# Performance work log

Measured on AMD Instinct MI355X. Metric: run time of the kernel, lower is better.

The kernel has to match this reference:

```python
import jax, jax.numpy as jnp
import numpy as np

LMAX = 6; MMAX = 2
C = 128          # num_channels
H = 8            # num_heads
ALPHA = 32       # attn_alpha_channels
VAL = 16         # attn_value_channels (H*VAL == C)
HID = 64         # attn_hidden_channels
FFN = 128        # ffn_hidden_channels
NL = 4           # num_layers
CUTOFF = 12.0; NRBF = 600
AVG_DEG = 23.395238876342773
AVG_NODES = 77.81317
EPS = 1e-16

def _maps():
    idx, ls = [], []
    for l in range(LMAX + 1):
        mm = min(l, MMAX)
        for m in range(-mm, mm + 1):
            idx.append(l * l + l + m); ls.append(l)
    return np.array(idx), np.array(ls)
_M2F_np, _LOF_np = _maps()
M2F = jnp.asarray(_M2F_np)   # [KM] full-coefficient index of each m-restricted coeff
LOF = jnp.asarray(_LOF_np)   # [KM] degree l of each m-restricted coeff
KM = int(_M2F_np.shape[0])   # 29 for lmax=6, mmax=2
KF = (LMAX + 1) ** 2         # 49

def _rbf(d):
    # GaussianSmearing(0, cutoff, NRBF, width_scalar=2.0)
    off = jnp.linspace(0.0, CUTOFF, NRBF)
    coeff = -0.5 / (2.0 * (off[1] - off[0])) ** 2
    return jnp.exp(coeff * (d[:, None] - off) ** 2)

def _envelope(d):
    # PolynomialEnvelope, exponent p=5
    x = d / CUTOFF
    env = 1.0 - 21.0 * x ** 5 + 35.0 * x ** 6 - 15.0 * x ** 7
    return jnp.where(x < 1.0, env, 0.0)

def _rms(x, g):
    # merge-norm over channel dim with learned per-channel scale
    return x * jax.lax.rsqrt(jnp.mean(x * x, axis=-1, keepdims=True) + 1e-6) * g

def _forward(atomic_numbers, edge_index, edge_distance, emb,
             We0, be0, We1, be1, Weproj, gamma1, gamma2,
             Wr0, Wr1, Wrl, Wmsg, Wap, wa, Wg, Wv, Wo,
             Wf1, Wfg, Wf2, Wh1, Wh2):
    N = atomic_numbers.shape[0]
    src, tgt = edge_index[0], edge_index[1]
    rbf = _rbf(edge_distance)            # [E, NRBF]
    env = _envelope(edge_distance)       # [E]
    # node init: atom embedding on the l=0 component
    x = jnp.zeros((N, KF, C), rbf.dtype).at[:, 0, :].set(emb[atomic_numbers])
    # edge-degree embedding: radial MLP -> per-edge coeffs -> scatter to targets
    h = jax.nn.silu(rbf @ We0 + be0)
    h = jax.nn.silu(h @ We1 + be1)
    deg = (h @ Weproj).reshape(-1, KM, C)              # [E, KM, C]
    x = x.at[tgt[:, None], M2F[None, :], :].add(deg / AVG_DEG)
    for i in range(NL):
        # ---- equivariant graph attention ----
        y = _rms(x, gamma1[i])
        ym = y[:, M2F, :]                               # [N, KM, C] m-restricted
        m = jnp.concatenate([ym[src], ym[tgt]], axis=-1)  # [E, KM, 2C]
        m = jnp.einsum('ekc,ch->ekh', m, Wmsg[i])       # [E, KM, HID]
        # radial function, shared across m within each l (use_rad_l_parametrization)
        rad = jax.nn.silu(jax.nn.silu(rbf @ Wr0[i]) @ Wr1[i])
        radl = rad @ Wrl[i]                             # [E, LMAX+1]
        m = m * radl[:, LOF][..., None]
        # attention logits from invariant (l=0) part
        a = jax.nn.silu(m[:, 0, :] @ Wap[i]).reshape(-1, H, ALPHA)
        logits = jnp.einsum('eha,ha->eh', a, wa[i])     # [E, H]
        segmax = jnp.full((N, H), -jnp.inf, logits.dtype).at[tgt].max(logits)
        ex = env[:, None] * jnp.exp(logits - segmax[tgt])  # envelope-masked softmax
        den = jax.ops.segment_sum(ex, tgt, num_segments=N)
        attn = ex / (den[tgt] + EPS)                    # [E, H]
        # SwiGLU-gated equivariant values
        g = jax.nn.silu(m[:, 0, :] @ Wg[i])             # [E, H*VAL]
        v = jnp.einsum('ekh,hv->ekv', m, Wv[i]) * g[:, None, :]
        v = v.reshape(-1, KM, H, VAL) * attn[:, None, :, None]
        agg = jax.ops.segment_sum(v.reshape(-1, KM, H * VAL), tgt, num_segments=N)
        out = jnp.einsum('nkv,vc->nkc', agg, Wo[i])     # [N, KM, C]
        x = x.at[:, M2F, :].add(out)
        # ---- feed-forward (grid-MLP style SwiGLU) ----
        y = _rms(x, gamma2[i])
        gf = jax.nn.silu(y[:, 0, :] @ Wfg[i])           # [N, FFN]
        hf = jnp.einsum('nkc,cf->nkf', y, Wf1[i]) * gf[:, None, :]
        x = x + jnp.einsum('nkf,fc->nkc', hf, Wf2[i])
    # energy head on invariant part, sum-aggregated over nodes
    s = jax.nn.silu(x[:, 0, :] @ Wh1) @ Wh2             # [N, 1]
    return (jnp.sum(s) / AVG_NODES).reshape(1)

def setup_inputs() -> dict:
    key = jax.random.key(0)
    ks = jax.random.split(key, 24)
    N, E = 6000, 120000
    def rn(k, shape, scale=0.05):
        return jax.random.normal(k, shape, dtype=jnp.float32) * scale
    inp = {}
    inp['atomic_numbers'] = jax.random.randint(ks[0], (N,), 0, 128)
    inp['edge_index'] = jax.random.randint(ks[1], (2, E), 0, N)
    inp['edge_distance'] = jax.random.uniform(ks[2], (E,), minval=0.5, maxval=CUTOFF, dtype=jnp.float32)
    inp['emb'] = rn(ks[3], (128, C), 1.0)
    inp['We0'] = rn(ks[4], (NRBF, 128)); inp['be0'] = jnp.zeros((128,), jnp.float32)
    inp['We1'] = rn(ks[5], (128, 128)); inp['be1'] = jnp.zeros((128,), jnp.float32)
    inp['Weproj'] = rn(ks[6], (128, KM * C))
    inp['gamma1'] = jnp.ones((NL, C), jnp.float32)
    inp['gamma2'] = jnp.ones((NL, C), jnp.float32)
    inp['Wr0'] = rn(ks[7], (NL, NRBF, 128))
    inp['Wr1'] = rn(ks[8], (NL, 128, 128))
    inp['Wrl'] = rn(ks[9], (NL, 128, LMAX + 1), 0.1)
    inp['Wmsg'] = rn(ks[10], (NL, 2 * C, HID))
    inp['Wap'] = rn(ks[11], (NL, HID, H * ALPHA))
    inp['wa'] = rn(ks[12], (NL, H, ALPHA))
    inp['Wg'] = rn(ks[13], (NL, HID, H * VAL))
    inp['Wv'] = rn(ks[14], (NL, HID, H * VAL))
    inp['Wo'] = rn(ks[15], (NL, H * VAL, C))
    inp['Wf1'] = rn(ks[16], (NL, C, FFN))
    inp['Wfg'] = rn(ks[17], (NL, C, FFN))
    inp['Wf2'] = rn(ks[18], (NL, FFN, C))
    inp['Wh1'] = rn(ks[19], (C, C))
    inp['Wh2'] = rn(ks[20], (C, 1))
    return inp

def reference(atomic_numbers, edge_index, edge_distance, emb,
              We0, be0, We1, be1, Weproj, gamma1, gamma2,
              Wr0, Wr1, Wrl, Wmsg, Wap, wa, Wg, Wv, Wo,
              Wf1, Wfg, Wf2, Wh1, Wh2):
    return _forward(atomic_numbers, edge_index, edge_distance, emb,
                    We0, be0, We1, be1, Weproj, gamma1, gamma2,
                    Wr0, Wr1, Wrl, Wmsg, Wap, wa, Wg, Wv, Wo,
                    Wf1, Wfg, Wf2, Wh1, Wh2)
```

## Files before the change

kernel.cpp:

```cpp
#include <hip/hip_runtime.h>

#define KM 29
#define GTAB 2048

typedef __bf16 bf16_t;
typedef __bf16 bf16x8 __attribute__((ext_vector_type(8)));
typedef __bf16 bf16x4 __attribute__((ext_vector_type(4)));
typedef __bf16 bf16x2 __attribute__((ext_vector_type(2)));
typedef float  f32x4  __attribute__((ext_vector_type(4)));
typedef float  f32x2  __attribute__((ext_vector_type(2)));

__device__ __forceinline__ float silu_f(float x){ return x / (1.0f + __expf(-x)); }

__device__ __forceinline__ float wave_reduce_sum(float v){
  #pragma unroll
  for (int s = 1; s < 64; s <<= 1) v += __shfl_xor(v, s);
  return v;
}

__device__ __forceinline__ constexpr int LOF2(int k){
  return (k<1)?0 : (k<4)?1 : (k<9)?2 : (k<14)?3 : (k<19)?4 : (k<24)?5 : 6;
}

__device__ __forceinline__ f32x4 mfma16(bf16x8 a, bf16x8 b, f32x4 c){
  return __builtin_amdgcn_mfma_f32_16x16x32_bf16(a, b, c, 0, 0, 0);
}

__device__ __forceinline__ float env_f(float d){
  float xx = d*(1.0f/12.0f);
  float x2 = xx*xx, x4 = x2*x2, x5 = x4*xx;
  float env = 1.0f - 21.0f*x5 + 35.0f*x5*xx - 15.0f*x5*x2;
  return (xx < 1.0f) ? env : 0.0f;
}

__global__ void k_count(const int* __restrict__ EI, int* __restrict__ cnt, int E){
  int e = blockIdx.x*256 + threadIdx.x;
  if (e < E) atomicAdd(&cnt[EI[E+e]], 1);
}

__global__ __launch_bounds__(1024) void k_scan(int* __restrict__ cnt, int* __restrict__ rowptr, int N){
  __shared__ int ts[1024];
  int t = threadIdx.x;
  int base = t*8;
  int loc[8]; int sum = 0;
  #pragma unroll
  for (int u = 0; u < 8; u++){ int idx = base+u; int v = (idx < N) ? cnt[idx] : 0; loc[u] = sum; sum += v; }
  ts[t] = sum; __syncthreads();
  for (int off = 1; off < 1024; off <<= 1){
    int v = (t >= off) ? ts[t-off] : 0;
    __syncthreads();
    ts[t] += v;
    __syncthreads();
  }
  int excl = ts[t] - sum;
  #pragma unroll
  for (int u = 0; u < 8; u++){
    int idx = base+u;
    if (idx < N){ int r = excl + loc[u]; rowptr[idx] = r; cnt[idx] = r; }
  }
  if (t == 1023) rowptr[N] = ts[1023];
}

__global__ void k_fill(const int* __restrict__ EI, int* __restrict__ cur, int* __restrict__ order, int E){
  int e = blockIdx.x*256 + threadIdx.x;
  if (e < E){ int pos = atomicAdd(&cur[EI[E+e]], 1); order[pos] = e; }
}

__global__ void k_sort(const int* __restrict__ rowptr, int* __restrict__ order, int N){
  int n = blockIdx.x*256 + threadIdx.x;
  if (n >= N) return;
  int rp = rowptr[n], re = rowptr[n+1];
  for (int a = rp+1; a < re; a++){
    int key = order[a]; int b = a-1;
    while (b >= rp && order[b] > key){ order[b+1] = order[b]; b--; }
    order[b+1] = key;
  }
}

__global__ void k_tr(const float* __restrict__ src, bf16_t* __restrict__ dst,
                     int L, int R, int C, int Lstr){
  int idx = blockIdx.x*256 + threadIdx.x;
  int total = L*R*C;
  if (idx >= total) return;
  int l = idx / (R*C); int rem = idx - l*(R*C);
  int r = rem / C; int c = rem - r*C;
  dst[((size_t)l*C + c)*R + r] = (bf16_t)src[(size_t)l*Lstr + (size_t)r*C + c];
}

__global__ void k_tr2(const float* __restrict__ src, bf16_t* __restrict__ dst){
  int idx = blockIdx.x*256 + threadIdx.x;
  if (idx >= 4*128*128) return;
  int l = idx >> 14; int j = (idx >> 7) & 127; int c = idx & 127;
  float v = (j < 64) ? src[(size_t)l*16384 + c*64 + j]
                     : src[(size_t)l*16384 + 8192 + c*64 + (j-64)];
  dst[idx] = (bf16_t)v;
}

__global__ __launch_bounds__(256) void k_tab_embed(
    const float* __restrict__ We0, const float* __restrict__ be0,
    const float* __restrict__ We1, const float* __restrict__ be1,
    const float* __restrict__ Wr0, const float* __restrict__ Wr1, const float* __restrict__ Wrl,
    float* __restrict__ h2tab, float* __restrict__ radtab)
{
  __shared__ float sb[4][640];
  const int wid = threadIdx.x >> 6, lane = threadIdx.x & 63;
  const int e = blockIdx.x*4 + wid;
  if (e >= GTAB) return;
  const float d = e * (12.0f/(GTAB-1));
  const float DLT = 12.0f/599.0f;
  const float CO  = -0.5f/((2.0f*DLT)*(2.0f*DLT));
  int jc = (int)(d/DLT + 0.5f);
  int j0 = jc - 16; if (j0 < 0) j0 = 0; if (j0 > 600-32) j0 = 600-32;
  float diff = d - (float)(j0+lane)*DLT;
  float gval = __expf(CO*diff*diff);
  float p[10];
  #pragma unroll
  for (int u = 0; u < 10; u++) p[u] = 0.f;
  const int c2 = 2*lane;
  for (int jj = 0; jj < 32; jj++){
    float gj = __shfl(gval, jj);
    int row = j0 + jj;
    const float2 w0 = *(const float2*)(We0 + row*128 + c2);
    p[0] += gj*w0.x; p[1] += gj*w0.y;
    #pragma unroll
    for (int i = 0; i < 4; i++){
      const float2 wr = *(const float2*)(Wr0 + ((size_t)i*600 + row)*128 + c2);
      p[2+2*i] += gj*wr.x; p[3+2*i] += gj*wr.y;
    }
  }
  sb[wid][c2]   = silu_f(p[0] + be0[c2]);
  sb[wid][c2+1] = silu_f(p[1] + be0[c2+1]);
  #pragma unroll
  for (int i = 0; i < 4; i++){
    sb[wid][128 + 128*i + c2]   = silu_f(p[2+2*i]);
    sb[wid][128 + 128*i + c2+1] = silu_f(p[3+2*i]);
  }
  float a0 = 0.f, a1 = 0.f;
  for (int c = 0; c < 128; c++){
    float hv = sb[wid][c];
    const float2 w = *(const float2*)(We1 + c*128 + c2);
    a0 += hv*w.x; a1 += hv*w.y;
  }
  a0 = silu_f(a0 + be1[c2]); a1 = silu_f(a1 + be1[c2+1]);
  h2tab[(size_t)e*128 + c2]     = a0;
  h2tab[(size_t)e*128 + c2 + 1] = a1;
  #pragma unroll
  for (int i = 0; i < 4; i++){
    float r0 = 0.f, r1 = 0.f;
    const float* W1 = Wr1 + (size_t)i*128*128;
    for (int c = 0; c < 128; c++){
      float rv = sb[wid][128 + 128*i + c];
      const float2 w = *(const float2*)(W1 + c*128 + c2);
      r0 += rv*w.x; r1 += rv*w.y;
    }
    r0 = silu_f(r0); r1 = silu_f(r1);
    const float* Wl = Wrl + (size_t)i*128*7;
    float pl[7];
    #pragma unroll
    for (int l = 0; l < 7; l++) pl[l] = r0*Wl[c2*7+l] + r1*Wl[(c2+1)*7+l];
    #pragma unroll
    for (int l = 0; l < 7; l++) pl[l] = wave_reduce_sum(pl[l]);
    if (lane == 0){
      #pragma unroll
      for (int l = 0; l < 7; l++) radtab[(size_t)e*28 + i*7 + l] = pl[l];
    }
  }
}

__global__ void k_h2e(const float* __restrict__ ed, const float* __restrict__ h2tab,
                      bf16_t* __restrict__ h2e, int E){
  int idx = blockIdx.x*256 + threadIdx.x;
  if (idx >= E*128) return;
  int e = idx >> 7, ch = idx & 127;
  float d = ed[e];
  float u = d * ((GTAB-1)/12.0f);
  int j = (int)u; if (j > GTAB-2) j = GTAB-2;
  float f = u - (float)j;
  float a = h2tab[(size_t)j*128 + ch], b = h2tab[(size_t)(j+1)*128 + ch];
  h2e[idx] = (bf16_t)(a + f*(b-a));
}

__global__ __launch_bounds__(256) void k_init_x(
    const int* __restrict__ Z, const float* __restrict__ emb,
    const bf16_t* __restrict__ WeprojT, const bf16_t* __restrict__ h2e,
    const int* __restrict__ rowptr, const int* __restrict__ order,
    bf16_t* __restrict__ Xb, int N)
{
  __shared__ bf16_t h2s[32*136];
  __shared__ int Zs[32];
  int n0 = blockIdx.x*32, t = threadIdx.x;
  int half = t >> 7, ch = t & 127;
  for (int pair = 0; pair < 16; pair++){
    int nn = pair*2 + half;
    int n = n0 + nn;
    float acc = 0.f;
    if (n < N){
      int rp = rowptr[n], deg = rowptr[n+1]-rp;
      for (int idx = 0; idx < deg; idx++){
        int e = order[rp+idx];
        acc += (float)h2e[(size_t)e*128 + ch];
      }
    }
    h2s[nn*136 + ch] = (bf16_t)acc;
  }
  if (t < 32) Zs[t] = (n0 + t < N) ? Z[n0+t] : 0;
  __syncthreads();
  int wid = t >> 6, lane = t & 63;
  int mtile = wid & 1;
  int row = mtile*16 + (lane & 15);
  int koff = (lane >> 4)*8;
  bf16x8 afr[4];
  #pragma unroll
  for (int kk = 0; kk < 4; kk++) afr[kk] = *(const bf16x8*)(h2s + row*136 + kk*32 + koff);
  for (int nt = (wid>>1); nt < 232; nt += 2){
    f32x4 acc = {0.f,0.f,0.f,0.f};
    int col = nt*16 + (lane & 15);
    #pragma unroll
    for (int kk = 0; kk < 4; kk++){
      bf16x8 b = *(const bf16x8*)(WeprojT + (size_t)col*128 + kk*32 + koff);
      acc = mfma16(afr[kk], b, acc);
    }
    #pragma unroll
    for (int r = 0; r < 4; r++){
      int r32 = mtile*16 + (lane>>4)*4 + r;
      int n = n0 + r32;
      if (n < N){
        float v = acc[r] * (1.0f/23.395238876342773f);
        if (col < 128) v += emb[(size_t)Zs[r32]*128 + col];
        Xb[(size_t)n*3712 + col] = (bf16_t)v;
      }
    }
  }
}

__global__ __launch_bounds__(512) void k_pqv(
    const bf16_t* __restrict__ Xb, const float* __restrict__ gamma1,
    const bf16_t* __restrict__ WmsgCT, const bf16_t* __restrict__ WvT,
    unsigned char* __restrict__ PV8, bf16_t* __restrict__ qmb,
    float* __restrict__ P0, float* __restrict__ Q0, int layer)
{
  __shared__ bf16_t ys16[32*136];
  __shared__ bf16_t pq16[32*136];
  int n = blockIdx.x, t = threadIdx.x;
  int wid = t >> 6, lane = t & 63;
  const float* g1 = gamma1 + layer*128;
  const bf16_t* xp = Xb + (size_t)n*3712;
  for (int k = wid; k < KM; k += 8){
    float x0 = (float)xp[k*128 + lane], x1 = (float)xp[k*128 + 64 + lane];
    float ss = wave_reduce_sum(x0*x0 + x1*x1);
    float sc = rsqrtf(ss*(1.0f/128.0f) + 1e-6f);
    ys16[k*136 + lane]      = (bf16_t)(x0*sc*g1[lane]);
    ys16[k*136 + 64 + lane] = (bf16_t)(x1*sc*g1[64+lane]);
  }
  for (int idx = t; idx < 3*136; idx += 512) ys16[29*136 + idx] = (bf16_t)0.f;
  __syncthreads();
  int mtile = wid >> 2;
  int row = mtile*16 + (lane & 15);
  int koff = (lane >> 4)*8;
  {
    const bf16_t* Bc = WmsgCT + (size_t)layer*16384;
    f32x4 acc[2] = {{0,0,0,0},{0,0,0,0}};
    #pragma unroll
    for (int kk = 0; kk < 128; kk += 32){
      bf16x8 a = *(const bf16x8*)(ys16 + row*136 + kk + koff);
      #pragma unroll
      for (int u = 0; u < 2; u++){
        int col = ((wid&3)*2+u)*16 + (lane & 15);
        bf16x8 b = *(const bf16x8*)(Bc + (size_t)col*128 + kk + koff);
        acc[u] = mfma16(a, b, acc[u]);
      }
    }
    #pragma unroll
    for (int u = 0; u < 2; u++){
      int col = ((wid&3)*2+u)*16 + (lane & 15);
      #pragma unroll
      for (int r = 0; r < 4; r++){
        int r32 = mtile*16 + (lane>>4)*4 + r;
        pq16[r32*136 + col] = (bf16_t)acc[u][r];
      }
      if (mtile == 0 && (lane>>4) == 0){
        float v = acc[u][0];
        if (col < 64) P0[(size_t)n*64 + col] = v;
        else          Q0[(size_t)n*64 + col - 64] = v;
      }
    }
  }
  __syncthreads();
  {
    const bf16_t* Bt = WvT + (size_t)layer*8192;
    f32x4 acc[2] = {{0,0,0,0},{0,0,0,0}};
    #pragma unroll
    for (int kk = 0; kk < 64; kk += 32){
      bf16x8 a = *(const bf16x8*)(pq16 + row*136 + kk + koff);
      #pragma unroll
      for (int u = 0; u < 2; u++){
        int col = ((wid&3)*2+u)*16 + (lane & 15);
        bf16x8 b = *(const bf16x8*)(Bt + (size_t)col*64 + kk + koff);
        acc[u] = mfma16(a, b, acc[u]);
      }
    }
    unsigned char* pvp = PV8 + (size_t)n*4096;
    int r0i = mtile*16 + (lane>>4)*4;
    #pragma unroll
    for (int u = 0; u < 2; u++){
      int col = ((wid&3)*2+u)*16 + (lane & 15);
      float pk[4];
      #pragma unroll
      for (int r = 0; r < 4; r++){
        int r32 = r0i + r;
        pk[r] = (r32 < KM) ? acc[u][r] : 0.f;
      }
      int dw = __builtin_amdgcn_cvt_pk_fp8_f32(pk[0], pk[1], 0, false);
      dw = __builtin_amdgcn_cvt_pk_fp8_f32(pk[2], pk[3], dw, true);
      *(unsigned int*)(pvp + col*32 + r0i) = (unsigned int)dw;
    }
  }
  for (int idx = t; idx < KM*64; idx += 512){
    int k = idx >> 6, j = idx & 63;
    qmb[(size_t)n*1856 + idx] = pq16[k*136 + 64 + j];
  }
}

__global__ __launch_bounds__(256) void k_edge_logits(
    const int* __restrict__ EI, const float* __restrict__ ed,
    const float* __restrict__ P0, const float* __restrict__ Q0,
    const float* __restrict__ radtab, const bf16_t* __restrict__ WapT, const float* __restrict__ wa,
    const bf16_t* __restrict__ WgT, float* __restrict__ logi, bf16_t* __restrict__ gate16,
    int E, int layer)
{
  __shared__ bf16_t m0s[16*72];
  __shared__ int   srcs[16], tgts[16];
  __shared__ float r0s[16];
  int t = threadIdx.x;
  int eb = blockIdx.x*16;
  if (t < 16){
    int e = eb + t;
    if (e < E){
      srcs[t] = EI[e]; tgts[t] = EI[E+e];
      float d = ed[e];
      float u = d * ((GTAB-1)/12.0f);
      int j = (int)u; if (j > GTAB-2) j = GTAB-2;
      float f = u - (float)j;
      float a = radtab[(size_t)j*28 + layer*7], b = radtab[(size_t)(j+1)*28 + layer*7];
      r0s[t] = a + f*(b-a);
    } else { srcs[t] = 0; tgts[t] = 0; r0s[t] = 0.f; }
  }
  __syncthreads();
  #pragma unroll
  for (int u = 0; u < 4; u++){
    int idx = t + u*256;
    int i = idx >> 6, j = idx & 63;
    m0s[i*72 + j] = (bf16_t)((P0[(size_t)srcs[i]*64 + j] + Q0[(size_t)tgts[i]*64 + j]) * r0s[i]);
  }
  __syncthreads();
  int wid = t >> 6, lane = t & 63;
  int l15 = lane & 15, lg = lane >> 4;
  int koff = lg*8;
  bf16x8 a0 = *(const bf16x8*)(m0s + l15*72 + koff);
  bf16x8 a1 = *(const bf16x8*)(m0s + l15*72 + 32 + koff);
  const bf16_t* Ba = WapT + (size_t)layer*16384;
  const bf16_t* Bg = WgT  + (size_t)layer*8192;
  const float* wav = wa + layer*256;
  f32x4 accA[4], accG[2];
  #pragma unroll
  for (int u = 0; u < 4; u++){
    int col = 64*wid + u*16 + l15;
    f32x4 acc = {0,0,0,0};
    acc = mfma16(a0, *(const bf16x8*)(Ba + (size_t)col*64 + koff), acc);
    acc = mfma16(a1, *(const bf16x8*)(Ba + (size_t)col*64 + 32 + koff), acc);
    accA[u] = acc;
  }
  #pragma unroll
  for (int u = 0; u < 2; u++){
    int col = 32*wid + u*16 + l15;
    f32x4 acc = {0,0,0,0};
    acc = mfma16(a0, *(const bf16x8*)(Bg + (size_t)col*64 + koff), acc);
    acc = mfma16(a1, *(const bf16x8*)(Bg + (size_t)col*64 + 32 + koff), acc);
    accG[u] = acc;
  }
  #pragma unroll
  for (int u = 0; u < 2; u++){
    int col = 32*wid + u*16 + l15;
    #pragma unroll
    for (int r = 0; r < 4; r++){
      int e = eb + lg*4 + r;
      if (e < E) gate16[(size_t)e*128 + col] = (bf16_t)silu_f(accG[u][r]);
    }
  }
  #pragma unroll
  for (int hpair = 0; hpair < 2; hpair++){
    int c0 = 64*wid + hpair*32 + l15;
    float w0 = wav[c0], w1 = wav[c0+16];
    float s[4];
    #pragma unroll
    for (int r = 0; r < 4; r++)
      s[r] = silu_f(accA[2*hpair][r])*w0 + silu_f(accA[2*hpair+1][r])*w1;
    #pragma unroll
    for (int r = 0; r < 4; r++){
      s[r] += __shfl_xor(s[r], 1);
      s[r] += __shfl_xor(s[r], 2);
      s[r] += __shfl_xor(s[r], 4);
      s[r] += __shfl_xor(s[r], 8);
    }
    if (l15 == 0){
      #pragma unroll
      for (int r = 0; r < 4; r++){
        int e = eb + lg*4 + r;
        if (e < E) logi[(size_t)e*8 + 2*wid + hpair] = s[r];
      }
    }
  }
}

#define FMA_DW(dw, kb) { \
  f32x2 lo_ = __builtin_amdgcn_cvt_pk_f32_fp8((dw), false); \
  f32x2 hi_ = __builtin_amdgcn_cvt_pk_f32_fp8((dw), true); \
  acc[(kb)]   += lo_.x * rw[LOF2((kb))]; \
  acc[(kb)+1] += lo_.y * rw[LOF2((kb)+1)]; \
  acc[(kb)+2] += hi_.x * rw[LOF2((kb)+2)]; \
  acc[(kb)+3] += hi_.y * rw[LOF2((kb)+3)]; }

__global__ __launch_bounds__(512, 4) void k_attn_ffn(
    const int* __restrict__ EI, const int* __restrict__ rowptr, const int* __restrict__ order,
    const float* __restrict__ ed, const bf16_t* __restrict__ qmb,
    const bf16_t* __restrict__ WvT, const bf16_t* __restrict__ WoT,
    const unsigned char* __restrict__ PV8, const bf16_t* __restrict__ gate16,
    const float* __restrict__ logi, const float* __restrict__ radtab,
    const float* __restrict__ gamma2, const float* __restrict__ Wfg,
    const bf16_t* __restrict__ Wf1T, const bf16_t* __restrict__ Wf2T,
    bf16_t* __restrict__ Xb, int layer,
    const float* __restrict__ gamma1, const bf16_t* __restrict__ WmsgCT,
    unsigned char* __restrict__ PV8o, bf16_t* __restrict__ qmbo,
    float* __restrict__ P0o, float* __restrict__ Q0o, int do_tail)
{
  __shared__ float  xs[3712];
  __shared__ bf16_t ysag[32*136];
  __shared__ bf16_t hsqv[32*136];
  __shared__ char   uA[4608];
  __shared__ float  mh[8], iden[8];

  bf16_t* qm16 = (bf16_t*)uA;
  float*  at8  = (float*)uA;
  float*  rl7  = (float*)(uA + 2048);
  int*    es   = (int*)(uA + 4096);
  int*    srcs = (int*)(uA + 4352);
  float*  pf   = (float*)uA;

  int n = blockIdx.x, t = threadIdx.x;
  int wid = t >> 6, lane = t & 63;
  int rp = rowptr[n], deg = rowptr[n+1] - rp;

  {
    const bf16x2* Xp2 = (const bf16x2*)(Xb + (size_t)n*3712);
    for (int p = t; p < 1856; p += 512){
      bf16x2 v = Xp2[p];
      xs[2*p]   = (float)v.x;
      xs[2*p+1] = (float)v.y;
    }
  }

  if (deg > 0){
    for (int idx = t; idx < KM*64; idx += 512){
      int k = idx >> 6, j = idx & 63;
      qm16[k*72 + j] = qmb[(size_t)n*1856 + idx];
    }
    for (int idx = t; idx < 3*72; idx += 512) qm16[29*72 + idx] = (bf16_t)0.f;
    if (t < 64){
      int hh = t & 7, slot = t >> 3;
      float m = -3.0e38f;
      for (int idx = slot; idx < deg; idx += 8){
        int e = order[rp+idx];
        m = fmaxf(m, logi[(size_t)e*8 + hh]);
      }
      m = fmaxf(m, __shfl_xor(m, 8));
      m = fmaxf(m, __shfl_xor(m, 16));
      m = fmaxf(m, __shfl_xor(m, 32));
      float den = 0.f;
      for (int idx = slot; idx < deg; idx += 8){
        int e = order[rp+idx];
        den += env_f(ed[e]) * __expf(logi[(size_t)e*8 + hh] - m);
      }
      den += __shfl_xor(den, 8);
      den += __shfl_xor(den, 16);
      den += __shfl_xor(den, 32);
      if (t < 8){ mh[t] = m; iden[t] = 1.0f/(den + 1e-16f); }
    }
    __syncthreads();
    {
      const bf16_t* Bt = WvT + (size_t)layer*8192;
      int mtile = wid >> 2, colt = (wid & 3)*2;
      int row = mtile*16 + (lane & 15);
      int koff = (lane >> 4)*8;
      f32x4 a2[2] = {{0,0,0,0},{0,0,0,0}};
      #pragma unroll
      for (int kk = 0; kk < 64; kk += 32){
        bf16x8 a = *(const bf16x8*)(qm16 + row*72 + kk + koff);
        #pragma unroll
        for (int u = 0; u < 2; u++){
          int col = (colt+u)*16 + (lane & 15);
          bf16x8 b = *(const bf16x8*)(Bt + (size_t)col*64 + kk + koff);
          a2[u] = mfma16(a, b, a2[u]);
        }
      }
      #pragma unroll
      for (int u = 0; u < 2; u++){
        int col = (colt+u)*16 + (lane & 15);
        #pragma unroll
        for (int r = 0; r < 4; r++){
          int r32 = mtile*16 + (lane>>4)*4 + r;
          hsqv[r32*136 + col] = (bf16_t)a2[u][r];
        }
      }
    }
    __syncthreads();
    int eg = t >> 7, hv = t & 127, h = hv >> 4;
    float acc[32];
    #pragma unroll
    for (int j = 0; j < 32; j++) acc[j] = 0.f;
    float S[7];
    #pragma unroll
    for (int l = 0; l < 7; l++) S[l] = 0.f;
    for (int base = 0; base < deg; base += 64){
      int ne = min(64, deg - base);
      if (t < ne){ int e = order[rp + base + t]; es[t] = e; srcs[t] = EI[e]; }
      __syncthreads();
      if (t < ne*8){
        int i = t >> 3, q = t & 7;
        int e = es[i];
        float d = ed[e];
        at8[t] = env_f(d) * __expf(logi[(size_t)e*8 + q] - mh[q]) * iden[q];
        if (q < 7){
          float u = d * ((GTAB-1)/12.0f);
          int j = (int)u; if (j > GTAB-2) j = GTAB-2;
          float f = u - (float)j;
          float a = radtab[(size_t)j*28 + layer*7 + q], b = radtab[(size_t)(j+1)*28 + layer*7 + q];
          rl7[t] = a + f*(b-a);
        }
      }
      __syncthreads();
      uint4 A0 = {0,0,0,0}, A1 = {0,0,0,0}, B0 = {0,0,0,0}, B1 = {0,0,0,0};
      float gA = 0.f, gB = 0.f;
      int i = eg;
      if (i < ne){
        const uint4* p = (const uint4*)(PV8 + (size_t)srcs[i]*4096 + hv*32);
        A0 = p[0]; A1 = p[1];
        gA = (float)gate16[(size_t)es[i]*128 + hv];
      }
      if (i + 4 < ne){
        const uint4* p = (const uint4*)(PV8 + (size_t)srcs[i+4]*4096 + hv*32);
        B0 = p[0]; B1 = p[1];
        gB = (float)gate16[(size_t)es[i+4]*128 + hv];
      }
      while (i < ne){
        int i2 = i + 8;
        uint4 C0 = {0,0,0,0}, C1 = {0,0,0,0}; float gC = 0.f;
        if (i2 < ne){
          const uint4* p = (const uint4*)(PV8 + (size_t)srcs[i2]*4096 + hv*32);
          C0 = p[0]; C1 = p[1];
          gC = (float)gate16[(size_t)es[i2]*128 + hv];
        }
        float w = gA * at8[i*8 + h];
        float rw[7];
        #pragma unroll
        for (int l = 0; l < 7; l++){ rw[l] = rl7[i*8 + l]*w; S[l] += rw[l]; }
        FMA_DW(A0.x, 0)  FMA_DW(A0.y, 4)  FMA_DW(A0.z, 8)  FMA_DW(A0.w, 12)
        FMA_DW(A1.x, 16) FMA_DW(A1.y, 20) FMA_DW(A1.z, 24) FMA_DW(A1.w, 28)
        A0 = B0; A1 = B1; gA = gB;
        B0 = C0; B1 = C1; gB = gC;
        i += 4;
      }
      __syncthreads();
    }
    #pragma unroll
    for (int j = 0; j < 32; j++)
      acc[j] += (float)hsqv[j*136 + hv] * S[LOF2(j)];
    __syncthreads();
    if (eg == 0){
      #pragma unroll
      for (int j = 0; j < 32; j++) ysag[j*136 + hv] = (bf16_t)acc[j];
    } else if (eg == 1){
      #pragma unroll
      for (int j = 0; j < 32; j++) hsqv[j*136 + hv] = (bf16_t)acc[j];
    }
    __syncthreads();
    if (eg == 2){
      #pragma unroll
      for (int j = 0; j < 32; j++) ysag[j*136 + hv] = (bf16_t)((float)ysag[j*136 + hv] + acc[j]);
    } else if (eg == 3){
      #pragma unroll
      for (int j = 0; j < 32; j++) hsqv[j*136 + hv] = (bf16_t)((float)hsqv[j*136 + hv] + acc[j]);
    }
    __syncthreads();
    for (int idx = t; idx < 32*128; idx += 512){
      int k = idx >> 7, c = idx & 127;
      ysag[k*136 + c] = (bf16_t)((float)ysag[k*136 + c] + (float)hsqv[k*136 + c]);
    }
    __syncthreads();
    {
      const bf16_t* Bt = WoT + (size_t)layer*16384;
      int mtile = wid >> 2, colt = (wid & 3)*2;
      int row = mtile*16 + (lane & 15);
      int koff = (lane >> 4)*8;
      f32x4 a2[2] = {{0,0,0,0},{0,0,0,0}};
      #pragma unroll
      for (int kk = 0; kk < 128; kk += 32){
        bf16x8 a = *(const bf16x8*)(ysag + row*136 + kk + koff);
        #pragma unroll
        for (int u = 0; u < 2; u++){
          int col = (colt+u)*16 + (lane & 15);
          bf16x8 b = *(const bf16x8*)(Bt + (size_t)col*128 + kk + koff);
          a2[u] = mfma16(a, b, a2[u]);
        }
      }
      #pragma unroll
      for (int u = 0; u < 2; u++){
        int col = (colt+u)*16 + (lane & 15);
        #pragma unroll
        for (int r = 0; r < 4; r++){
          int r32 = mtile*16 + (lane>>4)*4 + r;
          if (r32 < KM) xs[r32*128 + col] += a2[u][r];
        }
      }
    }
  }
  __syncthreads();
  const float* g2 = gamma2 + layer*128;
  for (int k = wid; k < KM; k += 8){
    float x0 = xs[k*128 + lane], x1 = xs[k*128 + 64 + lane];
    float ss = wave_reduce_sum(x0*x0 + x1*x1);
    float sc = rsqrtf(ss*(1.0f/128.0f) + 1e-6f);
    ysag[k*136 + lane]      = (bf16_t)(x0*sc*g2[lane]);
    ysag[k*136 + 64 + lane] = (bf16_t)(x1*sc*g2[64+lane]);
  }
  for (int idx = t; idx < 3*136; idx += 512) ysag[29*136 + idx] = (bf16_t)0.f;
  __syncthreads();
  {
    int part = t >> 7, f = t & 127;
    const float* Wfgp = Wfg + (size_t)layer*16384;
    float p = 0.f;
    for (int c = part*32; c < part*32 + 32; c++) p += (float)ysag[c] * Wfgp[c*128 + f];
    pf[part*128 + f] = p;
  }
  __syncthreads();
  if (t < 128) pf[512 + t] = silu_f(pf[t] + pf[128+t] + pf[256+t] + pf[384+t]);
  __syncthreads();
  {
    const bf16_t* Bt = Wf1T + (size_t)layer*16384;
    int mtile = wid >> 2, colt = (wid & 3)*2;
    int row = mtile*16 + (lane & 15);
    int koff = (lane >> 4)*8;
    f32x4 a2[2] = {{0,0,0,0},{0,0,0,0}};
    #pragma unroll
    for (int kk = 0; kk < 128; kk += 32){
      bf16x8 a = *(const bf16x8*)(ysag + row*136 + kk + koff);
      #pragma unroll
      for (int u = 0; u < 2; u++){
        int col = (colt+u)*16 + (lane & 15);
        bf16x8 b = *(const bf16x8*)(Bt + (size_t)col*128 + kk + koff);
        a2[u] = mfma16(a, b, a2[u]);
      }
    }
    #pragma unroll
    for (int u = 0; u < 2; u++){
      int col = (colt+u)*16 + (lane & 15);
      float gfc = pf[512 + col];
      #pragma unroll
      for (int r = 0; r < 4; r++){
        int r32 = mtile*16 + (lane>>4)*4 + r;
        hsqv[r32*136 + col] = (bf16_t)(a2[u][r]*gfc);
      }
    }
  }
  __syncthreads();
  {
    const bf16_t* Bt = Wf2T + (size_t)layer*16384;
    int mtile = wid >> 2, colt = (wid & 3)*2;
    int row = mtile*16 + (lane & 15);
    int koff = (lane >> 4)*8;
    f32x4 a2[2] = {{0,0,0,0},{0,0,0,0}};
    #pragma unroll
    for (int kk = 0; kk < 128; kk += 32){
      bf16x8 a = *(const bf16x8*)(hsqv + row*136 + kk + koff);
      #pragma unroll
      for (int u = 0; u < 2; u++){
        int col = (colt+u)*16 + (lane & 15);
        bf16x8 b = *(const bf16x8*)(Bt + (size_t)col*128 + kk + koff);
        a2[u] = mfma16(a, b, a2[u]);
      }
    }
    #pragma unroll
    for (int u = 0; u < 2; u++){
      int col = (colt+u)*16 + (lane & 15);
      #pragma unroll
      for (int r = 0; r < 4; r++){
        int r32 = mtile*16 + (lane>>4)*4 + r;
        if (r32 < KM) xs[r32*128 + col] += a2[u][r];
      }
    }
  }
  __syncthreads();
  {
    bf16x2* Xp2 = (bf16x2*)(Xb + (size_t)n*3712);
    for (int p = t; p < 1856; p += 512){
      bf16x2 v;
      v.x = (bf16_t)xs[2*p];
      v.y = (bf16_t)xs[2*p+1];
      Xp2[p] = v;
    }
  }
  if (do_tail){
    const float* g1n = gamma1 + (size_t)(layer+1)*128;
    for (int k = wid; k < KM; k += 8){
      float x0 = xs[k*128 + lane], x1 = xs[k*128 + 64 + lane];
      float ss = wave_reduce_sum(x0*x0 + x1*x1);
      float sc = rsqrtf(ss*(1.0f/128.0f) + 1e-6f);
      ysag[k*136 + lane]      = (bf16_t)(x0*sc*g1n[lane]);
      ysag[k*136 + 64 + lane] = (bf16_t)(x1*sc*g1n[64+lane]);
    }
    __syncthreads();
    int mtile = wid >> 2;
    int row = mtile*16 + (lane & 15);
    int koff = (lane >> 4)*8;
    {
      const bf16_t* Bc = WmsgCT + (size_t)(layer+1)*16384;
      f32x4 acc[2] = {{0,0,0,0},{0,0,0,0}};
      #pragma unroll
      for (int kk = 0; kk < 128; kk += 32){
        bf16x8 a = *(const bf16x8*)(ysag + row*136 + kk + koff);
        #pragma unroll
        for (int u = 0; u < 2; u++){
          int col = ((wid&3)*2+u)*16 + (lane & 15);
          bf16x8 b = *(const bf16x8*)(Bc + (size_t)col*128 + kk + koff);
          acc[u] = mfma16(a, b, acc[u]);
        }
      }
      #pragma unroll
      for (int u = 0; u < 2; u++){
        int col = ((wid&3)*2+u)*16 + (lane & 15);
        #pragma unroll
        for (int r = 0; r < 4; r++){
          int r32 = mtile*16 + (lane>>4)*4 + r;
          hsqv[r32*136 + col] = (bf16_t)acc[u][r];
        }
        if (mtile == 0 && (lane>>4) == 0){
          float v = acc[u][0];
          if (col < 64) P0o[(size_t)n*64 + col] = v;
          else          Q0o[(size_t)n*64 + col - 64] = v;
        }
      }
    }
    __syncthreads();
    {
      const bf16_t* Bt = WvT + (size_t)(layer+1)*8192;
      f32x4 acc[2] = {{0,0,0,0},{0,0,0,0}};
      #pragma unroll
      for (int kk = 0; kk < 64; kk += 32){
        bf16x8 a = *(const bf16x8*)(hsqv + row*136 + kk + koff);
        #pragma unroll
        for (int u = 0; u < 2; u++){
          int col = ((wid&3)*2+u)*16 + (lane & 15);
          bf16x8 b = *(const bf16x8*)(Bt + (size_t)col*64 + kk + koff);
          acc[u] = mfma16(a, b, acc[u]);
        }
      }
      unsigned char* pvp = PV8o + (size_t)n*4096;
      int r0i = mtile*16 + (lane>>4)*4;
      #pragma unroll
      for (int u = 0; u < 2; u++){
        int col = ((wid&3)*2+u)*16 + (lane & 15);
        float pk[4];
        #pragma unroll
        for (int r = 0; r < 4; r++){
          int r32 = r0i + r;
          pk[r] = (r32 < KM) ? acc[u][r] : 0.f;
        }
        int dw = __builtin_amdgcn_cvt_pk_fp8_f32(pk[0], pk[1], 0, false);
        dw = __builtin_amdgcn_cvt_pk_fp8_f32(pk[2], pk[3], dw, true);
        *(unsigned int*)(pvp + col*32 + r0i) = (unsigned int)dw;
      }
    }
    for (int idx = t; idx < KM*64; idx += 512){
      int k = idx >> 6, j = idx & 63;
      qmbo[(size_t)n*1856 + idx] = hsqv[k*136 + 64 + j];
    }
  }
}

__global__ __launch_bounds__(256) void k_head(
    const bf16_t* __restrict__ Xb, const float* __restrict__ Wh1, const float* __restrict__ Wh2,
    float* __restrict__ partial, int N)
{
  __shared__ float wsum[4];
  int t = threadIdx.x;
  int half = t >> 7;
  int n = blockIdx.x*2 + half;
  int f = t & 127;
  float sv = 0.f;
  if (n < N){
    const bf16_t* xp = Xb + (size_t)n*3712;
    float acc = 0.f;
    for (int c = 0; c < 128; c++) acc += (float)xp[c]*Wh1[c*128 + f];
    sv = silu_f(acc)*Wh2[f];
  }
  sv = wave_reduce_sum(sv);
  if ((t & 63) == 0) wsum[t >> 6] = sv;
  __syncthreads();
  if (t == 0) partial[blockIdx.x] = wsum[0] + wsum[1] + wsum[2] + wsum[3];
}

__global__ __launch_bounds__(256) void k_reduce(const float* __restrict__ partial, float* __restrict__ out, int P){
  __shared__ float sh[256];
  int t = threadIdx.x;
  float s = 0.f;
  for (int i = t; i < P; i += 256) s += partial[i];
  sh[t] = s; __syncthreads();
  for (int off = 128; off > 0; off >>= 1){
    if (t < off) sh[t] += sh[t+off];
    __syncthreads();
  }
  if (t == 0) out[0] = sh[0] / 77.81317f;
}

extern "C" void kernel_launch(void* const* d_in, const int* in_sizes, int n_in,
                              void* d_out, int out_size, void* d_ws, size_t ws_size,
                              hipStream_t stream)
{
  const int*   Z      = (const int*)d_in[0];
  const int*   EI     = (const int*)d_in[1];
  const float* ed     = (const float*)d_in[2];
  const float* emb    = (const float*)d_in[3];
  const float* We0    = (const float*)d_in[4];
  const float* be0    = (const float*)d_in[5];
  const float* We1    = (const float*)d_in[6];
  const float* be1    = (const float*)d_in[7];
  const float* Weproj = (const float*)d_in[8];
  const float* gamma1 = (const float*)d_in[9];
  const float* gamma2 = (const float*)d_in[10];
  const float* Wr0    = (const float*)d_in[11];
  const float* Wr1    = (const float*)d_in[12];
  const float* Wrl    = (const float*)d_in[13];
  const float* Wmsg   = (const float*)d_in[14];
  const float* Wap    = (const float*)d_in[15];
  const float* wa     = (const float*)d_in[16];
  const float* Wg     = (const float*)d_in[17];
  const float* Wv     = (const float*)d_in[18];
  const float* Wo     = (const float*)d_in[19];
  const float* Wf1    = (const float*)d_in[20];
  const float* Wfg    = (const float*)d_in[21];
  const float* Wf2    = (const float*)d_in[22];
  const float* Wh1    = (const float*)d_in[23];
  const float* Wh2    = (const float*)d_in[24];

  const int N = in_sizes[0];
  const int E = in_sizes[2];

  float* ws = (float*)d_ws;
  size_t o = 0;
  auto alloc = [&](size_t nf){ float* p = ws + o; o += (nf + 7) & ~(size_t)7; return p; };

  bf16_t* Xb    = (bf16_t*)alloc((size_t)N*1856);
  float* P0     = alloc((size_t)N*128);
  float* Q0     = alloc((size_t)N*128);
  float* logi   = alloc((size_t)E*8);
  float* part   = alloc((size_t)((N+1)/2) + 8);
  float* radtab = alloc((size_t)GTAB*28);
  bf16_t* qmb   = (bf16_t*)alloc((size_t)N*1856);
  float* h2tab  = (float*)qmb;
  unsigned char* PV8 = (unsigned char*)alloc((size_t)N*2048);
  bf16_t* gate16= (bf16_t*)alloc((size_t)E*64);
  bf16_t* arena = (bf16_t*)alloc(434176);
  int* rowptr = (int*)alloc((size_t)N+8);
  int* curs   = (int*)alloc((size_t)N);
  int* order  = (int*)alloc((size_t)E);

  bf16_t* WmsgCT  = arena;
  bf16_t* WvT     = arena + 65536;
  bf16_t* WoT     = arena + 98304;
  bf16_t* Wf1T    = arena + 163840;
  bf16_t* Wf2T    = arena + 229376;
  bf16_t* WapT    = arena + 294912;
  bf16_t* WgT     = arena + 360448;
  bf16_t* WeprojT = arena + 393216;

  bf16_t* h2e = gate16;

  hipMemsetAsync(curs, 0, sizeof(int)*N, stream);
  k_count<<<(E+255)/256, 256, 0, stream>>>(EI, curs, E);
  k_scan<<<1, 1024, 0, stream>>>(curs, rowptr, N);
  k_fill<<<(E+255)/256, 256, 0, stream>>>(EI, curs, order, E);
  k_sort<<<(N+255)/256, 256, 0, stream>>>(rowptr, order, N);

  k_tr2<<<256, 256, 0, stream>>>(Wmsg, WmsgCT);
  k_tr<<<128, 256, 0, stream>>>(Wv,   WvT,  4, 64, 128, 8192);
  k_tr<<<256, 256, 0, stream>>>(Wo,   WoT,  4, 128, 128, 16384);
  k_tr<<<256, 256, 0, stream>>>(Wf1,  Wf1T, 4, 128, 128, 16384);
  k_tr<<<256, 256, 0, stream>>>(Wf2,  Wf2T, 4, 128, 128, 16384);
  k_tr<<<256, 256, 0, stream>>>(Wap,  WapT, 4, 64, 256, 16384);
  k_tr<<<128, 256, 0, stream>>>(Wg,   WgT,  4, 64, 128, 8192);
  k_tr<<<1856, 256, 0, stream>>>(Weproj, WeprojT, 1, 128, 3712, 0);

  k_tab_embed<<<GTAB/4, 256, 0, stream>>>(We0, be0, We1, be1, Wr0, Wr1, Wrl, h2tab, radtab);
  k_h2e<<<(E*128+255)/256, 256, 0, stream>>>(ed, h2tab, h2e, E);
  k_init_x<<<(N+31)/32, 256, 0, stream>>>(Z, emb, WeprojT, h2e, rowptr, order, Xb, N);

  k_pqv<<<N, 512, 0, stream>>>(Xb, gamma1, WmsgCT, WvT, PV8, qmb, P0, Q0, 0);

  for (int i = 0; i < 4; i++){
    int cur = i & 1, nxt = (i+1) & 1;
    unsigned char* PV8i = PV8 + (size_t)cur*N*4096;
    unsigned char* PV8o = PV8 + (size_t)nxt*N*4096;
    bf16_t* qmbi = qmb + (size_t)cur*N*1856;
    bf16_t* qmbo = qmb + (size_t)nxt*N*1856;
    float* P0i = P0 + (size_t)cur*N*64, *P0o = P0 + (size_t)nxt*N*64;
    float* Q0i = Q0 + (size_t)cur*N*64, *Q0o = Q0 + (size_t)nxt*N*64;
    k_edge_logits<<<(E+15)/16, 256, 0, stream>>>(EI, ed, P0i, Q0i, radtab, WapT, wa, WgT, logi, gate16, E, i);
    k_attn_ffn<<<N, 512, 0, stream>>>(EI, rowptr, order, ed, qmbi, WvT, WoT, PV8i, gate16,
                                      logi, radtab, gamma2, Wfg, Wf1T, Wf2T, Xb, i,
                                      gamma1, WmsgCT, PV8o, qmbo, P0o, Q0o, (i < 3) ? 1 : 0);
  }

  int PB = (N+1)/2;
  k_head<<<PB, 256, 0, stream>>>(Xb, Wh1, Wh2, part, N);
  k_reduce<<<1, 256, 0, stream>>>(part, (float*)d_out, PB);
}
```

Baseline: 2.340 ms.

## Recompute query projection in attention kernel and drop separate softmax max pass

Stops storing the per-node query projection (qmb) to global memory. The attention kernel now recomputes it from the node features with an RMS-norm and a small MFMA GEMM. The softmax no longer subtracts a max and no longer makes a separate denominator pass: the denominator is accumulated during aggregation and applied afterward. Edge-index staging moves into dedicated shared arrays to remove per-chunk barriers, and the init-time neighbour sum is split into its own kernel for more parallelism. The trade-offs are extra compute per node and a risk of exp overflow without max subtraction.

```diff
diff --git a/kernel.cpp b/kernel.cpp
--- a/kernel.cpp
+++ b/kernel.cpp
@@ -180,28 +180,34 @@
   h2e[idx] = (bf16_t)(a + f*(b-a));
 }
 
+__global__ __launch_bounds__(256) void k_h2sum(
+    const bf16_t* __restrict__ h2e, const int* __restrict__ rowptr, const int* __restrict__ order,
+    bf16_t* __restrict__ h2sum, int N)
+{
+  int n = blockIdx.x*2 + (threadIdx.x >> 7);
+  int ch = threadIdx.x & 127;
+  if (n >= N) return;
+  int rp = rowptr[n], deg = rowptr[n+1] - rp;
+  float acc = 0.f;
+  for (int idx = 0; idx < deg; idx++){
+    int e = order[rp+idx];
+    acc += (float)h2e[(size_t)e*128 + ch];
+  }
+  h2sum[(size_t)n*128 + ch] = (bf16_t)acc;
+}
+
 __global__ __launch_bounds__(256) void k_init_x(
     const int* __restrict__ Z, const float* __restrict__ emb,
-    const bf16_t* __restrict__ WeprojT, const bf16_t* __restrict__ h2e,
-    const int* __restrict__ rowptr, const int* __restrict__ order,
+    const bf16_t* __restrict__ WeprojT, const bf16_t* __restrict__ h2sum,
     bf16_t* __restrict__ Xb, int N)
 {
   __shared__ bf16_t h2s[32*136];
   __shared__ int Zs[32];
   int n0 = blockIdx.x*32, t = threadIdx.x;
-  int half = t >> 7, ch = t & 127;
-  for (int pair = 0; pair < 16; pair++){
-    int nn = pair*2 + half;
+  for (int idx = t; idx < 32*128; idx += 256){
+    int nn = idx >> 7, ch = idx & 127;
     int n = n0 + nn;
-    float acc = 0.f;
-    if (n < N){
-      int rp = rowptr[n], deg = rowptr[n+1]-rp;
-      for (int idx = 0; idx < deg; idx++){
-        int e = order[rp+idx];
-        acc += (float)h2e[(size_t)e*128 + ch];
-      }
-    }
-    h2s[nn*136 + ch] = (bf16_t)acc;
+    h2s[nn*136 + ch] = (n < N) ? h2sum[(size_t)n*128 + ch] : (bf16_t)0.f;
   }
   if (t < 32) Zs[t] = (n0 + t < N) ? Z[n0+t] : 0;
   __syncthreads();
@@ -236,7 +242,7 @@
 __global__ __launch_bounds__(512) void k_pqv(
     const bf16_t* __restrict__ Xb, const float* __restrict__ gamma1,
     const bf16_t* __restrict__ WmsgCT, const bf16_t* __restrict__ WvT,
-    unsigned char* __restrict__ PV8, bf16_t* __restrict__ qmb,
+    unsigned char* __restrict__ PV8,
     float* __restrict__ P0, float* __restrict__ Q0, int layer)
 {
   __shared__ bf16_t ys16[32*136];
@@ -314,10 +320,6 @@
       dw = __builtin_amdgcn_cvt_pk_fp8_f32(pk[2], pk[3], dw, true);
       *(unsigned int*)(pvp + col*32 + r0i) = (unsigned int)dw;
     }
-  }
-  for (int idx = t; idx < KM*64; idx += 512){
-    int k = idx >> 6, j = idx & 63;
-    qmb[(size_t)n*1856 + idx] = pq16[k*136 + 64 + j];
   }
 }
 
@@ -422,28 +424,28 @@
 
 __global__ __launch_bounds__(512, 4) void k_attn_ffn(
     const int* __restrict__ EI, const int* __restrict__ rowptr, const int* __restrict__ order,
-    const float* __restrict__ ed, const bf16_t* __restrict__ qmb,
+    const float* __restrict__ ed,
     const bf16_t* __restrict__ WvT, const bf16_t* __restrict__ WoT,
     const unsigned char* __restrict__ PV8, const bf16_t* __restrict__ gate16,
     const float* __restrict__ logi, const float* __restrict__ radtab,
-    const float* __restrict__ gamma2, const float* __restrict__ Wfg,
+    const float* __restrict__ gamma1, const float* __restrict__ gamma2,
+    const float* __restrict__ Wfg,
     const bf16_t* __restrict__ Wf1T, const bf16_t* __restrict__ Wf2T,
+    const bf16_t* __restrict__ WmsgCT,
     bf16_t* __restrict__ Xb, int layer,
-    const float* __restrict__ gamma1, const bf16_t* __restrict__ WmsgCT,
-    unsigned char* __restrict__ PV8o, bf16_t* __restrict__ qmbo,
-    float* __restrict__ P0o, float* __restrict__ Q0o, int do_tail)
+    unsigned char* __restrict__ PV8o, float* __restrict__ P0o, float* __restrict__ Q0o,
+    int do_tail)
 {
   __shared__ float  xs[3712];
   __shared__ bf16_t ysag[32*136];
   __shared__ bf16_t hsqv[32*136];
   __shared__ char   uA[4608];
-  __shared__ float  mh[8], iden[8];
+  __shared__ int    esb[64], srcs[64];
+  __shared__ float  denl[32];
 
   bf16_t* qm16 = (bf16_t*)uA;
   float*  at8  = (float*)uA;
   float*  rl7  = (float*)(uA + 2048);
-  int*    es   = (int*)(uA + 4096);
-  int*    srcs = (int*)(uA + 4352);
   float*  pf   = (float*)uA;
 
   int n = blockIdx.x, t = threadIdx.x;
@@ -458,32 +460,43 @@
       xs[2*p+1] = (float)v.y;
     }
   }
+  {
+    int m0 = (deg < 64) ? deg : 64;
+    if (t < m0){ int e = order[rp + t]; esb[t] = e; srcs[t] = EI[e]; }
+  }
+  __syncthreads();
 
   if (deg > 0){
-    for (int idx = t; idx < KM*64; idx += 512){
-      int k = idx >> 6, j = idx & 63;
-      qm16[k*72 + j] = qmb[(size_t)n*1856 + idx];
-    }
-    for (int idx = t; idx < 3*72; idx += 512) qm16[29*72 + idx] = (bf16_t)0.f;
-    if (t < 64){
-      int hh = t & 7, slot = t >> 3;
-      float m = -3.0e38f;
-      for (int idx = slot; idx < deg; idx += 8){
-        int e = order[rp+idx];
-        m = fmaxf(m, logi[(size_t)e*8 + hh]);
-      }
-      m = fmaxf(m, __shfl_xor(m, 8));
-      m = fmaxf(m, __shfl_xor(m, 16));
-      m = fmaxf(m, __shfl_xor(m, 32));
-      float den = 0.f;
-      for (int idx = slot; idx < deg; idx += 8){
-        int e = order[rp+idx];
-        den += env_f(ed[e]) * __expf(logi[(size_t)e*8 + hh] - m);
-      }
-      den += __shfl_xor(den, 8);
-      den += __shfl_xor(den, 16);
-      den += __shfl_xor(den, 32);
-      if (t < 8){ mh[t] = m; iden[t] = 1.0f/(den + 1e-16f); }
+    {
+      const float* g1 = gamma1 + layer*128;
+      for (int k = wid; k < KM; k += 8){
+        float x0 = xs[k*128 + lane], x1 = xs[k*128 + 64 + lane];
+        float ss = wave_reduce_sum(x0*x0 + x1*x1);
+        float sc = rsqrtf(ss*(1.0f/128.0f) + 1e-6f);
+        ysag[k*136 + lane]      = (bf16_t)(x0*sc*g1[lane]);
+        ysag[k*136 + 64 + lane] = (bf16_t)(x1*sc*g1[64+lane]);
+      }
+      for (int idx = t; idx < 3*136; idx += 512) ysag[29*136 + idx] = (bf16_t)0.f;
+    }
+    __syncthreads();
+    {
+      const bf16_t* Bc = WmsgCT + (size_t)layer*16384 + (size_t)64*128;
+      int mtile = wid >> 2;
+      int col = (wid & 3)*16 + (lane & 15);
+      int row = mtile*16 + (lane & 15);
+      int koff = (lane >> 4)*8;
+      f32x4 a2 = {0,0,0,0};
+      #pragma unroll
+      for (int kk = 0; kk < 128; kk += 32){
+        bf16x8 a = *(const bf16x8*)(ysag + row*136 + kk + koff);
+        bf16x8 b = *(const bf16x8*)(Bc + (size_t)col*128 + kk + koff);
+        a2 = mfma16(a, b, a2);
+      }
+      #pragma unroll
+      for (int r = 0; r < 4; r++){
+        int r32 = mtile*16 + (lane>>4)*4 + r;
+        qm16[r32*72 + col] = (bf16_t)a2[r];
+      }
     }
     __syncthreads();
     {
@@ -520,15 +533,19 @@
     float S[7];
     #pragma unroll
     for (int l = 0; l < 7; l++) S[l] = 0.f;
+    float dpart = 0.f;
     for (int base = 0; base < deg; base += 64){
       int ne = min(64, deg - base);
-      if (t < ne){ int e = order[rp + base + t]; es[t] = e; srcs[t] = EI[e]; }
-      __syncthreads();
+      if (base > 0){
+        __syncthreads();
+        if (t < ne){ int e = order[rp + base + t]; esb[t] = e; srcs[t] = EI[e]; }
+        __syncthreads();
+      }
       if (t < ne*8){
         int i = t >> 3, q = t & 7;
-        int e = es[i];
+        int e = esb[i];
         float d = ed[e];
-        at8[t] = env_f(d) * __expf(logi[(size_t)e*8 + q] - mh[q]) * iden[q];
+        at8[t] = env_f(d) * __expf(logi[(size_t)e*8 + q]);
         if (q < 7){
           float u = d * ((GTAB-1)/12.0f);
           int j = (int)u; if (j > GTAB-2) j = GTAB-2;
@@ -544,12 +561,12 @@
       if (i < ne){
         const uint4* p = (const uint4*)(PV8 + (size_t)srcs[i]*4096 + hv*32);
         A0 = p[0]; A1 = p[1];
-        gA = (float)gate16[(size_t)es[i]*128 + hv];
+        gA = (float)gate16[(size_t)esb[i]*128 + hv];
       }
       if (i + 4 < ne){
         const uint4* p = (const uint4*)(PV8 + (size_t)srcs[i+4]*4096 + hv*32);
         B0 = p[0]; B1 = p[1];
-        gB = (float)gate16[(size_t)es[i+4]*128 + hv];
+        gB = (float)gate16[(size_t)esb[i+4]*128 + hv];
       }
       while (i < ne){
         int i2 = i + 8;
@@ -557,9 +574,11 @@
         if (i2 < ne){
           const uint4* p = (const uint4*)(PV8 + (size_t)srcs[i2]*4096 + hv*32);
           C0 = p[0]; C1 = p[1];
-          gC = (float)gate16[(size_t)es[i2]*128 + hv];
-        }
-        float w = gA * at8[i*8 + h];
+          gC = (float)gate16[(size_t)esb[i2]*128 + hv];
+        }
+        float ae = at8[i*8 + h];
+        dpart += ae;
+        float w = gA * ae;
         float rw[7];
         #pragma unroll
         for (int l = 0; l < 7; l++){ rw[l] = rl7[i*8 + l]*w; S[l] += rw[l]; }
@@ -569,12 +588,18 @@
         B0 = C0; B1 = C1; gB = gC;
         i += 4;
       }
-      __syncthreads();
     }
     #pragma unroll
     for (int j = 0; j < 32; j++)
       acc[j] += (float)hsqv[j*136 + hv] * S[LOF2(j)];
-    __syncthreads();
+    if ((hv & 15) == 0) denl[eg*8 + h] = dpart;
+    __syncthreads();
+    {
+      float dsum = denl[h] + denl[8 + h] + denl[16 + h] + denl[24 + h];
+      float inv = 1.0f/(dsum + 1e-30f);
+      #pragma unroll
+      for (int j = 0; j < 32; j++) acc[j] *= inv;
+    }
     if (eg == 0){
       #pragma unroll
       for (int j = 0; j < 32; j++) ysag[j*136 + hv] = (bf16_t)acc[j];
@@ -778,10 +803,6 @@
         dw = __builtin_amdgcn_cvt_pk_fp8_f32(pk[2], pk[3], dw, true);
         *(unsigned int*)(pvp + col*32 + r0i) = (unsigned int)dw;
       }
-    }
-    for (int idx = t; idx < KM*64; idx += 512){
-      int k = idx >> 6, j = idx & 63;
-      qmbo[(size_t)n*1856 + idx] = hsqv[k*136 + 64 + j];
     }
   }
 }
@@ -864,8 +885,8 @@
   float* logi   = alloc((size_t)E*8);
   float* part   = alloc((size_t)((N+1)/2) + 8);
   float* radtab = alloc((size_t)GTAB*28);
-  bf16_t* qmb   = (bf16_t*)alloc((size_t)N*1856);
-  float* h2tab  = (float*)qmb;
+  float* h2tab  = alloc((size_t)GTAB*128);
+  bf16_t* h2sum = (bf16_t*)alloc((size_t)N*64);
   unsigned char* PV8 = (unsigned char*)alloc((size_t)N*2048);
   bf16_t* gate16= (bf16_t*)alloc((size_t)E*64);
   bf16_t* arena = (bf16_t*)alloc(434176);
@@ -901,22 +922,21 @@
 
   k_tab_embed<<<GTAB/4, 256, 0, stream>>>(We0, be0, We1, be1, Wr0, Wr1, Wrl, h2tab, radtab);
   k_h2e<<<(E*128+255)/256, 256, 0, stream>>>(ed, h2tab, h2e, E);
-  k_init_x<<<(N+31)/32, 256, 0, stream>>>(Z, emb, WeprojT, h2e, rowptr, order, Xb, N);
-
-  k_pqv<<<N, 512, 0, stream>>>(Xb, gamma1, WmsgCT, WvT, PV8, qmb, P0, Q0, 0);
+  k_h2sum<<<(N+1)/2, 256, 0, stream>>>(h2e, rowptr, order, h2sum, N);
+  k_init_x<<<(N+31)/32, 256, 0, stream>>>(Z, emb, WeprojT, h2sum, Xb, N);
+
+  k_pqv<<<N, 512, 0, stream>>>(Xb, gamma1, WmsgCT, WvT, PV8, P0, Q0, 0);
 
   for (int i = 0; i < 4; i++){
     int cur = i & 1, nxt = (i+1) & 1;
     unsigned char* PV8i = PV8 + (size_t)cur*N*4096;
     unsigned char* PV8o = PV8 + (size_t)nxt*N*4096;
-    bf16_t* qmbi = qmb + (size_t)cur*N*1856;
-    bf16_t* qmbo = qmb + (size_t)nxt*N*1856;
     float* P0i = P0 + (size_t)cur*N*64, *P0o = P0 + (size_t)nxt*N*64;
     float* Q0i = Q0 + (size_t)cur*N*64, *Q0o = Q0 + (size_t)nxt*N*64;
     k_edge_logits<<<(E+15)/16, 256, 0, stream>>>(EI, ed, P0i, Q0i, radtab, WapT, wa, WgT, logi, gate16, E, i);
-    k_attn_ffn<<<N, 512, 0, stream>>>(EI, rowptr, order, ed, qmbi, WvT, WoT, PV8i, gate16,
-                                      logi, radtab, gamma2, Wfg, Wf1T, Wf2T, Xb, i,
-                                      gamma1, WmsgCT, PV8o, qmbo, P0o, Q0o, (i < 3) ? 1 : 0);
+    k_attn_ffn<<<N, 512, 0, stream>>>(EI, rowptr, order, ed, WvT, WoT, PV8i, gate16,
+                                      logi, radtab, gamma1, gamma2, Wfg, Wf1T, Wf2T, WmsgCT,
+                                      Xb, i, PV8o, P0o, Q0o, (i < 3) ? 1 : 0);
   }
 
   int PB = (N+1)/2;
```

New measurement: 2.211 ms. -5.5%, faster.
